# Performance work log

Hardware: AMD Instinct MI355X
Metric: run time of the kernel (lower is better)

The kernel has to match this reference:

```python
import jax, jax.numpy as jnp
import numpy as np

N_FFT = 2048
HOP = 512
N_FREQ = N_FFT // 2 + 1  # 1025


def _dft_conv_weights():
    # periodic ('fftbins=True') Hann window, matching librosa get_window('hann', N, fftbins=True)
    n = np.arange(N_FFT)
    win = 0.5 - 0.5 * np.cos(2.0 * np.pi * n / N_FFT)
    k = np.arange(N_FREQ)
    ang = 2.0 * np.pi * np.outer(k, n) / N_FFT  # (F, n_fft)
    # W[n, k] = exp(-2*pi*i*n*k/N); real part = cos, imag part = -sin; windowed per-tap
    w_real = (np.cos(ang) * win[None, :]).astype(np.float32)
    w_imag = (-np.sin(ang) * win[None, :]).astype(np.float32)
    return w_real, w_imag


def setup_inputs() -> dict:
    key = jax.random.key(0)
    x = jax.random.normal(key, (16, 320000), dtype=jnp.float32)
    w_real, w_imag = _dft_conv_weights()
    return {
        "input": x,
        "conv_real_w": jnp.asarray(w_real),
        "conv_imag_w": jnp.asarray(w_imag),
    }


def reference(input, conv_real_w, conv_imag_w):
    # center=True: reflect-pad n_fft//2 on both sides
    pad = N_FFT // 2
    x = jnp.pad(input, ((0, 0), (pad, pad)), mode="reflect")  # (B, L + n_fft)
    L = x.shape[1]
    T = (L - N_FFT) // HOP + 1  # time_steps
    # frame extraction == Conv1d with kernel n_fft, stride hop
    idx = jnp.arange(T)[:, None] * HOP + jnp.arange(N_FFT)[None, :]  # (T, n_fft)
    frames = x[:, idx]  # (B, T, n_fft)
    real = jnp.einsum("btn,fn->bft", frames, conv_real_w)  # (B, F, T)
    imag = jnp.einsum("btn,fn->bft", frames, conv_imag_w)  # (B, F, T)
    return real, imag
```

## Files before the change

### kernel.cpp

```cpp
#include <hip/hip_runtime.h>

#define B_BATCH 16
#define XLEN    320000
#define NFFT    2048
#define HOP     512
#define PADW    1024
#define NFREQ   1025
#define T_OUT   626
#define M_ROWS  2050
#define NCOLS   (B_BATCH * T_OUT)
#define BM      128
#define BN      256
#define BK      64
#define MT2     17
#define NT2     40
#define KT2     32

#define XPAD_LEN    322048
#define XPAD_STRIDE 330240
#define APACK_BYTES ((size_t)MT2 * KT2 * 2 * 8192)
#define XPAD_BYTES  ((size_t)(B_BATCH + 1) * XPAD_STRIDE * 2)
#define WS_NEEDED   (APACK_BYTES + XPAD_BYTES)

typedef __bf16 bf16x8 __attribute__((ext_vector_type(8)));
typedef __bf16 bf16x4 __attribute__((ext_vector_type(4)));
typedef float  f32x4  __attribute__((ext_vector_type(4)));

__device__ __forceinline__ void gload_lds16(const void* g, void* l) {
    __builtin_amdgcn_global_load_lds(
        (const __attribute__((address_space(1))) unsigned int*)g,
        (__attribute__((address_space(3))) unsigned int*)l,
        16, 0, 0);
}

__global__ __launch_bounds__(256) void prep_w(
    const float* __restrict__ wre, const float* __restrict__ wim,
    __bf16* __restrict__ apack)
{
    const int gid  = blockIdx.x * 256 + threadIdx.x;
    const int scell = gid & 3;
    const int row   = (gid >> 2) & 127;
    const int ks    = (gid >> 9) & 1;
    const int kt    = (gid >> 10) & 31;
    const int mt    = gid >> 15;

    const int grow = mt * 128 + row;
    const int k    = kt * 64 + ks * 32 + ((scell ^ (row & 3)) << 3);

    bf16x8 v = bf16x8{};
    if (grow < M_ROWS) {
        const float* src = (grow < NFREQ)
            ? (wre + (size_t)grow * NFFT + k)
            : (wim + (size_t)(grow - NFREQ) * NFFT + k);
        const float4 a = *reinterpret_cast<const float4*>(src);
        const float4 b = *reinterpret_cast<const float4*>(src + 4);
        v[0] = (__bf16)a.x; v[1] = (__bf16)a.y; v[2] = (__bf16)a.z; v[3] = (__bf16)a.w;
        v[4] = (__bf16)b.x; v[5] = (__bf16)b.y; v[6] = (__bf16)b.z; v[7] = (__bf16)b.w;
    }
    *reinterpret_cast<bf16x8*>(apack + (size_t)gid * 8) = v;
}

__global__ __launch_bounds__(256) void prep_x(
    const float* __restrict__ x, __bf16* __restrict__ xpad)
{
    const int gid = blockIdx.x * 256 + threadIdx.x;
    if (gid >= (B_BATCH + 1) * (XPAD_STRIDE / 8)) return;
    const int b  = gid / (XPAD_STRIDE / 8);
    const int i0 = (gid - b * (XPAD_STRIDE / 8)) * 8;

    bf16x8 v = bf16x8{};
    if (b < B_BATCH) {
        const float* xb = x + (size_t)b * XLEN;
        const int pos0 = i0 - PADW;
        if (pos0 >= 0 && pos0 + 8 <= XLEN) {
            const float4 a = *reinterpret_cast<const float4*>(xb + pos0);
            const float4 c = *reinterpret_cast<const float4*>(xb + pos0 + 4);
            v[0] = (__bf16)a.x; v[1] = (__bf16)a.y; v[2] = (__bf16)a.z; v[3] = (__bf16)a.w;
            v[4] = (__bf16)c.x; v[5] = (__bf16)c.y; v[6] = (__bf16)c.z; v[7] = (__bf16)c.w;
        } else {
            #pragma unroll
            for (int e = 0; e < 8; ++e) {
                const int i = i0 + e;
                if (i >= XPAD_LEN) { v[e] = (__bf16)0.f; continue; }
                int p = i - PADW;
                p = (p < 0) ? -p : p;
                p = (p >= XLEN) ? (2 * XLEN - 2 - p) : p;
                v[e] = (__bf16)xb[p];
            }
        }
    }
    *reinterpret_cast<bf16x8*>(xpad + (size_t)b * XPAD_STRIDE + i0) = v;
}


#define MFMA16 __builtin_amdgcn_mfma_f32_16x16x32_bf16

#define PH(BUF, KS, STAGE, VMW) do {                                              \
    const unsigned abase = (unsigned)(((BUF)*2+(KS)) << 13) + offA_base;          \
    const unsigned bbase = (unsigned)(((BUF)*2+(KS)) << 14) + offB_base;          \
    bf16x8 a0 = *(const bf16x8*)(lds + abase);                                    \
    bf16x8 a1 = *(const bf16x8*)(lds + abase + 1024);                             \
    bf16x8 a2 = *(const bf16x8*)(lds + abase + 2048);                             \
    bf16x8 a3 = *(const bf16x8*)(lds + abase + 3072);                             \
    bf16x8 b0 = *(const bf16x8*)(lds + bbase);                                    \
    bf16x8 b1 = *(const bf16x8*)(lds + bbase + 1024);                             \
    bf16x8 b2 = *(const bf16x8*)(lds + bbase + 2048);                             \
    bf16x8 b3 = *(const bf16x8*)(lds + bbase + 3072);                             \
    STAGE                                                                          \
    VMW                                                                            \
    __builtin_amdgcn_s_barrier();                                                  \
    __builtin_amdgcn_s_setprio(1);                                                 \
    acc[0][0] = MFMA16(a0, b0, acc[0][0], 0, 0, 0);                                \
    acc[0][1] = MFMA16(a0, b1, acc[0][1], 0, 0, 0);                                \
    acc[0][2] = MFMA16(a0, b2, acc[0][2], 0, 0, 0);                                \
    acc[0][3] = MFMA16(a0, b3, acc[0][3], 0, 0, 0);                                \
    acc[1][0] = MFMA16(a1, b0, acc[1][0], 0, 0, 0);                                \
    acc[1][1] = MFMA16(a1, b1, acc[1][1], 0, 0, 0);                                \
    acc[1][2] = MFMA16(a1, b2, acc[1][2], 0, 0, 0);                                \
    acc[1][3] = MFMA16(a1, b3, acc[1][3], 0, 0, 0);                                \
    acc[2][0] = MFMA16(a2, b0, acc[2][0], 0, 0, 0);                                \
    acc[2][1] = MFMA16(a2, b1, acc[2][1], 0, 0, 0);                                \
    acc[2][2] = MFMA16(a2, b2, acc[2][2], 0, 0, 0);                                \
    acc[2][3] = MFMA16(a2, b3, acc[2][3], 0, 0, 0);                                \
    acc[3][0] = MFMA16(a3, b0, acc[3][0], 0, 0, 0);                                \
    acc[3][1] = MFMA16(a3, b1, acc[3][1], 0, 0, 0);                                \
    acc[3][2] = MFMA16(a3, b2, acc[3][2], 0, 0, 0);                                \
    acc[3][3] = MFMA16(a3, b3, acc[3][3], 0, 0, 0);                                \
    __builtin_amdgcn_s_setprio(0);                                                 \
    __builtin_amdgcn_s_barrier();                                                  \
    __builtin_amdgcn_sched_barrier(0);                                             \
} while (0)

#define VM3 asm volatile("s_waitcnt vmcnt(3)" ::: "memory");
#define VM0 asm volatile("s_waitcnt vmcnt(0)" ::: "memory");

__global__ __launch_bounds__(512, 2) void stft_gemm3(
    const __bf16* __restrict__ apack,
    const __bf16* __restrict__ xpad,
    float* __restrict__ out)
{
    __shared__ __align__(16) unsigned char lds[98304];

    const int tid  = threadIdx.x;
    const int lane = tid & 63;
    const int wid  = tid >> 6;
    const int wm   = wid >> 2;
    const int wn   = wid & 3;
    const int fr   = lane & 15;
    const int kq   = lane >> 4;

    const int orig = (blockIdx.x & 7) * 85 + (blockIdx.x >> 3);
    const int nt = orig / MT2;
    const int mt = orig % MT2;

    const char* ablk = (const char*)apack + ((size_t)mt * KT2 * 2) * 8192 + (size_t)tid * 16;

    const char* xpb = (const char*)xpad;
    const int c0 = tid, c1 = tid + 512;
    const char* gb0;
    const char* gb1;
    {
        int row = c0 >> 2;
        int col = nt * 256 + row;
        unsigned b = (unsigned)col / 626u;
        int tc = col - (int)b * 626;
        int kqv = (c0 & 3) ^ (row & 3);
        gb0 = xpb + ((size_t)b * XPAD_STRIDE + (size_t)tc * 512) * 2 + kqv * 16;
        row = c1 >> 2;
        col = nt * 256 + row;
        b = (unsigned)col / 626u;
        tc = col - (int)b * 626;
        kqv = (c1 & 3) ^ (row & 3);
        gb1 = xpb + ((size_t)b * XPAD_STRIDE + (size_t)tc * 512) * 2 + kqv * 16;
    }

    auto stageA = [&](int kt, int ks, int buf) {
        gload_lds16(ablk + ((size_t)(kt * 2 + ks) << 13),
                    lds + ((buf * 2 + ks) << 13) + (wid << 10));
    };
    auto stageB = [&](int kt, int ks, int buf) {
        const int koff = kt * 128 + ks * 64;
        unsigned char* d = lds + 32768 + ((buf * 2 + ks) << 14) + (wid << 10);
        gload_lds16(gb0 + koff, d);
        gload_lds16(gb1 + koff, d + 8192);
    };

    const unsigned swz = (unsigned)(((kq ^ fr) & 3) << 4);
    const unsigned offA_base = (unsigned)((wm * 64 + fr) * 64) + swz;
    const unsigned offB_base = 32768u + (unsigned)((wn * 64 + fr) * 64) + swz;

    f32x4 acc[4][4];
    #pragma unroll
    for (int m = 0; m < 4; ++m)
        #pragma unroll
        for (int n = 0; n < 4; ++n)
            acc[m][n] = f32x4{0.f, 0.f, 0.f, 0.f};

    stageA(0, 0, 0); stageB(0, 0, 0);
    stageA(0, 1, 0); stageB(0, 1, 0);
    stageA(1, 0, 1); stageB(1, 0, 1);
    VM3
    __builtin_amdgcn_s_barrier();
    __builtin_amdgcn_sched_barrier(0);

    #pragma unroll 1
    for (int i = 0; i < 15; ++i) {
        const int t0 = 2 * i;
        PH(0, 0, stageA(t0 + 1, 1, 1); stageB(t0 + 1, 1, 1);, );
        PH(0, 1, stageA(t0 + 2, 0, 0); stageB(t0 + 2, 0, 0);, VM3);
        PH(1, 0, stageA(t0 + 2, 1, 0); stageB(t0 + 2, 1, 0);, );
        PH(1, 1, stageA(t0 + 3, 0, 1); stageB(t0 + 3, 0, 1);, VM3);
    }
    PH(0, 0, stageA(31, 1, 1); stageB(31, 1, 1);, );
    PH(0, 1, , VM0);
    PH(1, 0, , );
    PH(1, 1, , );

    const size_t imag_base = (size_t)B_BATCH * NFREQ * T_OUT;
    #pragma unroll
    for (int n = 0; n < 4; ++n) {
        const int col = nt * 256 + wn * 64 + n * 16 + fr;
        if (col < NCOLS) {
            const unsigned b = (unsigned)col / 626u;
            const int tc = col - (int)b * 626;
            const size_t colbase = (size_t)b * NFREQ * T_OUT + (size_t)tc;
            #pragma unroll
            for (int m = 0; m < 4; ++m) {
                #pragma unroll
                for (int j = 0; j < 4; ++j) {
                    const int grow = mt * 128 + wm * 64 + m * 16 + kq * 4 + j;
                    if (grow < M_ROWS) {
                        const size_t off = (grow < NFREQ)
                            ? colbase + (size_t)grow * T_OUT
                            : imag_base + colbase + (size_t)(grow - NFREQ) * T_OUT;
                        out[off] = acc[m][n][j];
                    }
                }
            }
        }
    }
}

__device__ __forceinline__ unsigned lds_off_fb(int row, int kbyte) {
    return (unsigned)(row * 128 + (kbyte ^ ((row & 7) << 4)));
}

__global__ __launch_bounds__(256) void stft_gemm_fb(
    const float* __restrict__ x,
    const float* __restrict__ wre,
    const float* __restrict__ wim,
    float* __restrict__ out)
{
    __shared__ __align__(16) unsigned char ldsA[128 * 128];
    __shared__ __align__(16) unsigned char ldsB[128 * 128];

    const int tid  = threadIdx.x;
    const int lane = tid & 63;
    const int wid  = tid >> 6;
    const int wmf  = wid >> 1;
    const int wnf  = wid & 1;

    const int bid = blockIdx.x;
    const int b   = bid / (17 * 5);
    const int rem = bid % (17 * 5);
    const int mt  = rem / 5;
    const int nt  = rem % 5;

    const int row0 = mt * 128;
    const int col0 = nt * 128;
    const float* xb = x + (size_t)b * XLEN;

    const int c4 = (tid & 15) * 4;
    const int r0 = tid >> 4;

    f32x4 acc[4][4];
    #pragma unroll
    for (int m = 0; m < 4; ++m)
        #pragma unroll
        for (int n = 0; n < 4; ++n)
            acc[m][n] = f32x4{0.f, 0.f, 0.f, 0.f};

    const int fr = lane & 15;
    const int kq = lane >> 4;

    for (int k0 = 0; k0 < NFFT; k0 += 64) {
        bf16x4 sa[8], sb[8];
        #pragma unroll
        for (int rr = 0; rr < 8; ++rr) {
            const int row  = rr * 16 + r0;
            const int grow = row0 + row;
            float4 v = make_float4(0.f, 0.f, 0.f, 0.f);
            if (grow < M_ROWS) {
                const float* wsrc = (grow < NFREQ)
                    ? (wre + (size_t)grow * NFFT)
                    : (wim + (size_t)(grow - NFREQ) * NFFT);
                v = *reinterpret_cast<const float4*>(wsrc + k0 + c4);
            }
            sa[rr].x = (__bf16)v.x; sa[rr].y = (__bf16)v.y;
            sa[rr].z = (__bf16)v.z; sa[rr].w = (__bf16)v.w;
        }
        #pragma unroll
        for (int rr = 0; rr < 8; ++rr) {
            const int trow = rr * 16 + r0;
            const int t    = col0 + trow;
            float4 v = make_float4(0.f, 0.f, 0.f, 0.f);
            if (t < T_OUT) {
                const int pos = t * HOP + k0 + c4 - PADW;
                if (pos >= 0 && pos <= XLEN - 4) {
                    v = *reinterpret_cast<const float4*>(xb + pos);
                } else {
                    float tmp[4];
                    #pragma unroll
                    for (int e = 0; e < 4; ++e) {
                        int p = pos + e;
                        p = (p < 0) ? -p : p;
                        p = (p >= XLEN) ? (2 * XLEN - 2 - p) : p;
                        tmp[e] = xb[p];
                    }
                    v = make_float4(tmp[0], tmp[1], tmp[2], tmp[3]);
                }
            }
            sb[rr].x = (__bf16)v.x; sb[rr].y = (__bf16)v.y;
            sb[rr].z = (__bf16)v.z; sb[rr].w = (__bf16)v.w;
        }
        __syncthreads();
        #pragma unroll
        for (int rr = 0; rr < 8; ++rr) {
            const int row = rr * 16 + r0;
            *reinterpret_cast<bf16x4*>(ldsA + lds_off_fb(row, c4 * 2)) = sa[rr];
            *reinterpret_cast<bf16x4*>(ldsB + lds_off_fb(row, c4 * 2)) = sb[rr];
        }
        __syncthreads();
        #pragma unroll
        for (int kk = 0; kk < 2; ++kk) {
            const int kbyte = kk * 64 + kq * 16;
            bf16x8 af[4], bfv[4];
            #pragma unroll
            for (int m = 0; m < 4; ++m)
                af[m] = *reinterpret_cast<const bf16x8*>(
                    ldsA + lds_off_fb(wmf * 64 + m * 16 + fr, kbyte));
            #pragma unroll
            for (int n = 0; n < 4; ++n)
                bfv[n] = *reinterpret_cast<const bf16x8*>(
                    ldsB + lds_off_fb(wnf * 64 + n * 16 + fr, kbyte));
            #pragma unroll
            for (int m = 0; m < 4; ++m)
                #pragma unroll
                for (int n = 0; n < 4; ++n)
                    acc[m][n] = MFMA16(af[m], bfv[n], acc[m][n], 0, 0, 0);
        }
    }

    const size_t imag_base = (size_t)B_BATCH * NFREQ * T_OUT;
    #pragma unroll
    for (int m = 0; m < 4; ++m) {
        #pragma unroll
        for (int n = 0; n < 4; ++n) {
            #pragma unroll
            for (int j = 0; j < 4; ++j) {
                const int grow = row0 + wmf * 64 + m * 16 + kq * 4 + j;
                const int gcol = col0 + wnf * 64 + n * 16 + fr;
                if (grow < M_ROWS && gcol < T_OUT) {
                    size_t off;
                    if (grow < NFREQ)
                        off = ((size_t)b * NFREQ + grow) * T_OUT + gcol;
                    else
                        off = imag_base + ((size_t)b * NFREQ + (grow - NFREQ)) * T_OUT + gcol;
                    out[off] = acc[m][n][j];
                }
            }
        }
    }
}

extern "C" void kernel_launch(void* const* d_in, const int* in_sizes, int n_in,
                              void* d_out, int out_size, void* d_ws, size_t ws_size,
                              hipStream_t stream) {
    const float* x   = (const float*)d_in[0];
    const float* wre = (const float*)d_in[1];
    const float* wim = (const float*)d_in[2];
    float* out = (float*)d_out;

    if (ws_size < WS_NEEDED) {
        stft_gemm_fb<<<dim3(B_BATCH * 17 * 5), 256, 0, stream>>>(x, wre, wim, out);
        return;
    }

    __bf16* apack = (__bf16*)d_ws;
    __bf16* xpad  = (__bf16*)((char*)d_ws + APACK_BYTES);

    prep_w<<<dim3(557056 / 256), 256, 0, stream>>>(wre, wim, apack);
    prep_x<<<dim3(((B_BATCH + 1) * (XPAD_STRIDE / 8) + 255) / 256), 256, 0, stream>>>(x, xpad);
    stft_gemm3<<<dim3(MT2 * NT2), 512, 0, stream>>>(apack, xpad, out);
}
```

Baseline: 135.8 us.

## Switch GEMM K-loop to a three-slot LDS ring with one barrier per phase

Replaces the two-buffer, two-substage LDS pipeline (96 KB) with a three-slot rotating ring (72 KB). Each phase now issues one wait and one barrier before reading, instead of a barrier on each side of the MFMA block. The LDS bank swizzle changes to XOR with row>>1, updated consistently in prep_w and the B-tile address setup, and launch bounds ask for 4 blocks per CU. The smaller LDS footprint should let more blocks stay resident per CU and cut barrier stalls. The cost is shallower prefetch depth, and the tighter occupancy hint may force register spills given the 64-float accumulator tile.

```diff
diff --git a/kernel.cpp b/kernel.cpp
--- a/kernel.cpp
+++ b/kernel.cpp
@@ -9,9 +9,6 @@
 #define T_OUT   626
 #define M_ROWS  2050
 #define NCOLS   (B_BATCH * T_OUT)
-#define BM      128
-#define BN      256
-#define BK      64
 #define MT2     17
 #define NT2     40
 #define KT2     32
@@ -37,7 +34,7 @@
     const float* __restrict__ wre, const float* __restrict__ wim,
     __bf16* __restrict__ apack)
 {
-    const int gid  = blockIdx.x * 256 + threadIdx.x;
+    const int gid   = blockIdx.x * 256 + threadIdx.x;
     const int scell = gid & 3;
     const int row   = (gid >> 2) & 127;
     const int ks    = (gid >> 9) & 1;
@@ -45,7 +42,7 @@
     const int mt    = gid >> 15;
 
     const int grow = mt * 128 + row;
-    const int k    = kt * 64 + ks * 32 + ((scell ^ (row & 3)) << 3);
+    const int k    = kt * 64 + ks * 32 + (((scell ^ (row >> 1)) & 3) << 3);
 
     bf16x8 v = bf16x8{};
     if (grow < M_ROWS) {
@@ -95,20 +92,35 @@
 
 #define MFMA16 __builtin_amdgcn_mfma_f32_16x16x32_bf16
 
-#define PH(BUF, KS, STAGE, VMW) do {                                              \
-    const unsigned abase = (unsigned)(((BUF)*2+(KS)) << 13) + offA_base;          \
-    const unsigned bbase = (unsigned)(((BUF)*2+(KS)) << 14) + offB_base;          \
-    bf16x8 a0 = *(const bf16x8*)(lds + abase);                                    \
-    bf16x8 a1 = *(const bf16x8*)(lds + abase + 1024);                             \
-    bf16x8 a2 = *(const bf16x8*)(lds + abase + 2048);                             \
-    bf16x8 a3 = *(const bf16x8*)(lds + abase + 3072);                             \
-    bf16x8 b0 = *(const bf16x8*)(lds + bbase);                                    \
-    bf16x8 b1 = *(const bf16x8*)(lds + bbase + 1024);                             \
-    bf16x8 b2 = *(const bf16x8*)(lds + bbase + 2048);                             \
-    bf16x8 b3 = *(const bf16x8*)(lds + bbase + 3072);                             \
-    STAGE                                                                          \
-    VMW                                                                            \
+#define VM3 asm volatile("s_waitcnt vmcnt(3)" ::: "memory");
+#define VM0 asm volatile("s_waitcnt vmcnt(0)" ::: "memory");
+
+#define STG(KT_, KS_, SLOT_) do {                                                  \
+    gload_lds16(ablk + (((KT_) * 2 + (KS_)) << 13),                                \
+                lds + ((SLOT_) << 13) + (wid << 10));                              \
+    {                                                                              \
+        const int koff = (KT_) * 128 + (KS_) * 64;                                 \
+        unsigned char* d_ = lds + 24576 + ((SLOT_) << 14) + (wid << 10);           \
+        gload_lds16(gb0 + koff, d_);                                               \
+        gload_lds16(gb1 + koff, d_ + 8192);                                        \
+    }                                                                              \
+} while (0)
+
+#define PH3(SLOT_, STAGE_, VMW_) do {                                              \
+    VMW_                                                                           \
     __builtin_amdgcn_s_barrier();                                                  \
+    __builtin_amdgcn_sched_barrier(0);                                             \
+    const unsigned abase = ((SLOT_) << 13) + offA_base;                            \
+    const unsigned bbase = 24576u + ((SLOT_) << 14) + offB_base;                   \
+    bf16x8 a0 = *(const bf16x8*)(lds + abase);                                     \
+    bf16x8 a1 = *(const bf16x8*)(lds + abase + 1024);                              \
+    bf16x8 a2 = *(const bf16x8*)(lds + abase + 2048);                              \
+    bf16x8 a3 = *(const bf16x8*)(lds + abase + 3072);                              \
+    bf16x8 b0 = *(const bf16x8*)(lds + bbase);                                     \
+    bf16x8 b1 = *(const bf16x8*)(lds + bbase + 1024);                              \
+    bf16x8 b2 = *(const bf16x8*)(lds + bbase + 2048);                              \
+    bf16x8 b3 = *(const bf16x8*)(lds + bbase + 3072);                              \
+    STAGE_                                                                         \
     __builtin_amdgcn_s_setprio(1);                                                 \
     acc[0][0] = MFMA16(a0, b0, acc[0][0], 0, 0, 0);                                \
     acc[0][1] = MFMA16(a0, b1, acc[0][1], 0, 0, 0);                                \
@@ -127,19 +139,14 @@
     acc[3][2] = MFMA16(a3, b2, acc[3][2], 0, 0, 0);                                \
     acc[3][3] = MFMA16(a3, b3, acc[3][3], 0, 0, 0);                                \
     __builtin_amdgcn_s_setprio(0);                                                 \
-    __builtin_amdgcn_s_barrier();                                                  \
-    __builtin_amdgcn_sched_barrier(0);                                             \
 } while (0)
 
-#define VM3 asm volatile("s_waitcnt vmcnt(3)" ::: "memory");
-#define VM0 asm volatile("s_waitcnt vmcnt(0)" ::: "memory");
-
-__global__ __launch_bounds__(512, 2) void stft_gemm3(
+__global__ __launch_bounds__(512, 4) void stft_gemm4(
     const __bf16* __restrict__ apack,
     const __bf16* __restrict__ xpad,
     float* __restrict__ out)
 {
-    __shared__ __align__(16) unsigned char lds[98304];
+    __shared__ __align__(16) unsigned char lds[73728];
 
     const int tid  = threadIdx.x;
     const int lane = tid & 63;
@@ -153,41 +160,27 @@
     const int nt = orig / MT2;
     const int mt = orig % MT2;
 
-    const char* ablk = (const char*)apack + ((size_t)mt * KT2 * 2) * 8192 + (size_t)tid * 16;
+    const char* ablk = (const char*)apack + (size_t)mt * (KT2 * 2 * 8192) + (size_t)tid * 16;
 
     const char* xpb = (const char*)xpad;
-    const int c0 = tid, c1 = tid + 512;
     const char* gb0;
     const char* gb1;
     {
-        int row = c0 >> 2;
-        int col = nt * 256 + row;
+        const int row0 = tid >> 2;
+        const int sc   = ((tid & 3) ^ (row0 >> 1)) & 3;
+        int col = nt * 256 + row0;
         unsigned b = (unsigned)col / 626u;
         int tc = col - (int)b * 626;
-        int kqv = (c0 & 3) ^ (row & 3);
-        gb0 = xpb + ((size_t)b * XPAD_STRIDE + (size_t)tc * 512) * 2 + kqv * 16;
-        row = c1 >> 2;
-        col = nt * 256 + row;
+        gb0 = xpb + ((size_t)b * XPAD_STRIDE + (size_t)tc * 512) * 2 + sc * 16;
+        col = nt * 256 + 128 + row0;
         b = (unsigned)col / 626u;
         tc = col - (int)b * 626;
-        kqv = (c1 & 3) ^ (row & 3);
-        gb1 = xpb + ((size_t)b * XPAD_STRIDE + (size_t)tc * 512) * 2 + kqv * 16;
-    }
-
-    auto stageA = [&](int kt, int ks, int buf) {
-        gload_lds16(ablk + ((size_t)(kt * 2 + ks) << 13),
-                    lds + ((buf * 2 + ks) << 13) + (wid << 10));
-    };
-    auto stageB = [&](int kt, int ks, int buf) {
-        const int koff = kt * 128 + ks * 64;
-        unsigned char* d = lds + 32768 + ((buf * 2 + ks) << 14) + (wid << 10);
-        gload_lds16(gb0 + koff, d);
-        gload_lds16(gb1 + koff, d + 8192);
-    };
-
-    const unsigned swz = (unsigned)(((kq ^ fr) & 3) << 4);
+        gb1 = xpb + ((size_t)b * XPAD_STRIDE + (size_t)tc * 512) * 2 + sc * 16;
+    }
+
+    const unsigned swz = (unsigned)(((kq ^ (fr >> 1)) & 3) << 4);
     const unsigned offA_base = (unsigned)((wm * 64 + fr) * 64) + swz;
-    const unsigned offB_base = 32768u + (unsigned)((wn * 64 + fr) * 64) + swz;
+    const unsigned offB_base = (unsigned)((wn * 64 + fr) * 64) + swz;
 
     f32x4 acc[4][4];
     #pragma unroll
@@ -196,25 +189,23 @@
         for (int n = 0; n < 4; ++n)
             acc[m][n] = f32x4{0.f, 0.f, 0.f, 0.f};
 
-    stageA(0, 0, 0); stageB(0, 0, 0);
-    stageA(0, 1, 0); stageB(0, 1, 0);
-    stageA(1, 0, 1); stageB(1, 0, 1);
-    VM3
-    __builtin_amdgcn_s_barrier();
-    __builtin_amdgcn_sched_barrier(0);
+    STG(0, 0, 0);
+    STG(0, 1, 1);
 
     #pragma unroll 1
-    for (int i = 0; i < 15; ++i) {
-        const int t0 = 2 * i;
-        PH(0, 0, stageA(t0 + 1, 1, 1); stageB(t0 + 1, 1, 1);, );
-        PH(0, 1, stageA(t0 + 2, 0, 0); stageB(t0 + 2, 0, 0);, VM3);
-        PH(1, 0, stageA(t0 + 2, 1, 0); stageB(t0 + 2, 1, 0);, );
-        PH(1, 1, stageA(t0 + 3, 0, 1); stageB(t0 + 3, 0, 1);, VM3);
-    }
-    PH(0, 0, stageA(31, 1, 1); stageB(31, 1, 1);, );
-    PH(0, 1, , VM0);
-    PH(1, 0, , );
-    PH(1, 1, , );
+    for (int i = 0; i < 10; ++i) {
+        const int kb = 3 * i;
+        PH3(0, STG(kb + 1, 0, 2);, VM3);
+        PH3(1, STG(kb + 1, 1, 0);, VM3);
+        PH3(2, STG(kb + 2, 0, 1);, VM3);
+        PH3(0, STG(kb + 2, 1, 2);, VM3);
+        PH3(1, STG(kb + 3, 0, 0);, VM3);
+        PH3(2, STG(kb + 3, 1, 1);, VM3);
+    }
+    PH3(0, STG(31, 0, 2);, VM3);
+    PH3(1, STG(31, 1, 0);, VM3);
+    PH3(2, , VM3);
+    PH3(0, , VM0);
 
     const size_t imag_base = (size_t)B_BATCH * NFREQ * T_OUT;
     #pragma unroll
@@ -391,5 +382,5 @@
 
     prep_w<<<dim3(557056 / 256), 256, 0, stream>>>(wre, wim, apack);
     prep_x<<<dim3(((B_BATCH + 1) * (XPAD_STRIDE / 8) + 255) / 256), 256, 0, stream>>>(x, xpad);
-    stft_gemm3<<<dim3(MT2 * NT2), 512, 0, stream>>>(apack, xpad, out);
-}
+    stft_gemm4<<<dim3(MT2 * NT2), 512, 0, stream>>>(apack, xpad, out);
+}
```

After: 112.9 us. -16.9%, faster.
